# Performance work log

Measured on AMD Instinct MI355X. Metric: run time of the kernel, lower is better.

Reference implementation:

```python
import jax, jax.numpy as jnp
import numpy as np

_LN2 = 0.6931471805599453
B, N, C, R, K = 256, 4096, 256, 32, 128
MAX_SPAN = 20.0
W_WEIGHT, W_COACT, W_SPAN = 1.0, 1.0, 0.3


def setup_inputs() -> dict:
    key = jax.random.key(0)
    k1, k2, k3, k4, k5 = jax.random.split(key, 5)
    A = jax.random.normal(k1, (B, N), dtype=jnp.float32)            # accumulated atom activations
    span_t = jax.random.uniform(k2, (B,), dtype=jnp.float32) * MAX_SPAN
    proto_weights = jax.random.normal(k3, (C, N), dtype=jnp.float32) * 0.5
    proto_coact_U = jax.random.normal(k4, (C, N, R), dtype=jnp.float32) * 0.1
    proto_span = jax.random.normal(k5, (C,), dtype=jnp.float32) + 5.0
    return {"A": A, "span_t": span_t, "proto_weights": proto_weights,
            "proto_coact_U": proto_coact_U, "proto_span": proto_span}


def reference(A, span_t, proto_weights, proto_coact_U, proto_span):
    # CoActivationComputer._compute: top-K atoms per trajectory
    topk_vals, topk_idx = jax.lax.top_k(A, K)                       # [B,K], [B,K]

    # --- match_score ---
    proto_w = jax.nn.softplus(proto_weights) - _LN2                 # [C,N]
    score_w = A @ proto_w.T                                          # [B,C]
    score_w = score_w - jnp.mean(score_w, axis=1, keepdims=True)

    # CoActState.frob_inner_lowrank: gather U rows at top-k indices
    U_t = jnp.transpose(proto_coact_U, (1, 2, 0))                    # [N,R,C]
    U_topk = U_t[topk_idx]                                           # [B,K,R,C] (irregular gather)
    Au = jnp.einsum('bk,bkrc->brc', topk_vals, U_topk)               # [B,R,C]
    score_coact = jnp.sum(Au ** 2, axis=1) / (K * R + 1e-9)          # [B,C]

    span_norm = jnp.clip(span_t / MAX_SPAN, 0.0, 1.0)                # [B]
    proto_span_norm = jax.nn.sigmoid(proto_span)                     # [C]
    score_span = -jnp.abs(span_norm[:, None] - proto_span_norm[None, :])

    match_scores = W_WEIGHT * score_w + W_COACT * score_coact + W_SPAN * score_span  # [B,C]

    # --- compute_residual_score ---
    beta = jax.nn.softmax(match_scores, axis=-1)                     # [B,C]
    U_recon = jnp.einsum('bc,cnr->bnr', beta, proto_coact_U)         # [B,N,R]
    norm_Mhat = jnp.sum(topk_vals ** 2, axis=1)                      # [B]
    U_recon_topk = jnp.take_along_axis(U_recon, topk_idx[:, :, None], axis=1)  # [B,K,R]
    Au2 = jnp.einsum('bk,bkr->br', topk_vals, U_recon_topk)          # [B,R]
    cross = jnp.sum(Au2 ** 2, axis=1) / (K * R + 1e-9)
    norm_Mrecon = jnp.sum(U_recon ** 2, axis=(1, 2)) / (K * R + 1e-9)
    norm_Mhat_n = norm_Mhat / (K + 1e-9)
    residual = jnp.clip(norm_Mhat_n - 2.0 * cross + norm_Mrecon, 0.0, 10000.0)  # [B]
    return residual
```

## Files before the change

kernel.cpp:

```cpp
#include <hip/hip_runtime.h>
#include <math.h>

#define Bb 256
#define Nn 4096
#define Cc 256
#define Rr 32
#define Kk 128
#define Lflat (Nn * Rr)
#define LN2f 0.6931471805599453f
#define SKW 16

typedef unsigned short u16;
typedef __attribute__((ext_vector_type(8))) short short8b;
typedef __attribute__((ext_vector_type(4))) float f32x4;

typedef __attribute__((address_space(1))) const void* gas_t;
typedef __attribute__((address_space(3))) void* las_t;
__device__ __forceinline__ void gll16(const void* g, void* l) {
  __builtin_amdgcn_global_load_lds((gas_t)g, (las_t)l, 16, 0, 0);
}

__device__ inline u16 f2bf(float x) {
  unsigned u = __float_as_uint(x);
  unsigned r = (u + 0x7fffu + ((u >> 16) & 1u)) >> 16;
  return (u16)r;
}

__device__ inline unsigned f2u(float f) {
  unsigned b = __float_as_uint(f);
  return (b & 0x80000000u) ? ~b : (b | 0x80000000u);
}
__device__ inline float u2f(unsigned u) {
  unsigned b = (u & 0x80000000u) ? (u ^ 0x80000000u) : ~u;
  return __uint_as_float(b);
}

__global__ __launch_bounds__(256) void topk_kernel(const float* __restrict__ A,
                                                   u16* __restrict__ S,
                                                   float* __restrict__ mhat) {
  int b = blockIdx.x, t = threadIdx.x;
  int lane = t & 63, wave = t >> 6;
  const float* row = A + (size_t)b * Nn;
  u16* Srow = S + (size_t)b * Nn;
  short8b z = {0, 0, 0, 0, 0, 0, 0, 0};
  *(short8b*)(Srow + t * 16) = z;
  *(short8b*)(Srow + t * 16 + 8) = z;

  float f[16]; unsigned u[16];
#pragma unroll
  for (int j = 0; j < 4; ++j) {
    float4 v = ((const float4*)row)[j * 256 + t];
    f[j * 4 + 0] = v.x; f[j * 4 + 1] = v.y; f[j * 4 + 2] = v.z; f[j * 4 + 3] = v.w;
  }
#pragma unroll
  for (int j = 0; j < 16; ++j) u[j] = f2u(f[j]);

  __shared__ int hist[4][256];
  __shared__ int sufs[257];
  __shared__ int wtot[4];
  __shared__ int s_d, s_cg;
  __shared__ int s_eqidx[256];
  __shared__ int s_eqcnt;
  __shared__ float redQ[4];
  if (t == 0) s_eqcnt = 0;

  unsigned T = 0u;
  int cntG = 0;
#pragma unroll
  for (int p = 3; p >= 0; --p) {
    hist[0][t] = 0; hist[1][t] = 0; hist[2][t] = 0; hist[3][t] = 0;
    __syncthreads();
    unsigned mh = (p == 3) ? 0u : (0xFFFFFFFFu << (8 * (p + 1)));
    int* hw = hist[wave];
#pragma unroll
    for (int j = 0; j < 16; ++j)
      if (((u[j] ^ T) & mh) == 0) atomicAdd(&hw[(u[j] >> (8 * p)) & 255], 1);
    __syncthreads();
    int v = hist[0][t] + hist[1][t] + hist[2][t] + hist[3][t];
#pragma unroll
    for (int off = 1; off < 64; off <<= 1) {
      int tmp = __shfl_down(v, off, 64);
      if (lane + off < 64) v += tmp;
    }
    if (lane == 0) wtot[wave] = v;
    __syncthreads();
    for (int w2 = wave + 1; w2 < 4; ++w2) v += wtot[w2];
    sufs[t] = v;
    if (t == 0) sufs[256] = 0;
    __syncthreads();
    int nxt = sufs[t + 1];
    if ((cntG + v >= Kk) && (cntG + nxt < Kk)) { s_d = t; s_cg = cntG + nxt; }
    __syncthreads();
    T |= (unsigned)s_d << (8 * p);
    cntG = s_cg;
    __syncthreads();
  }
  float sq = 0.f;
#pragma unroll
  for (int j = 0; j < 16; ++j) {
    int idx = (j >> 2) * 1024 + t * 4 + (j & 3);
    if (u[j] > T) {
      Srow[idx] = f2bf(f[j]);
      sq += f[j] * f[j];
    } else if (u[j] == T) {
      int q2 = atomicAdd(&s_eqcnt, 1);
      if (q2 < 256) s_eqidx[q2] = idx;
    }
  }
#pragma unroll
  for (int off = 32; off; off >>= 1) sq += __shfl_xor(sq, off, 64);
  if (lane == 0) redQ[wave] = sq;
  __syncthreads();
  if (t == 0) {
    float tv = u2f(T);
    u16 tb = f2bf(tv);
    int need = Kk - cntG;
    int eq = min(s_eqcnt, 256);
    for (int s2 = 0; s2 < need; ++s2) {
      int best = 0x7fffffff, bi = 0;
      for (int jj = 0; jj < eq; ++jj)
        if (s_eqidx[jj] < best) { best = s_eqidx[jj]; bi = jj; }
      Srow[best] = tb;
      s_eqidx[bi] = 0x7fffffff;
    }
    mhat[b] = redQ[0] + redQ[1] + redQ[2] + redQ[3] + (float)need * tv * tv;
  }
}

__global__ __launch_bounds__(256) void u2t_kernel(const float* __restrict__ U,
                                                  u16* __restrict__ UT) {
  int c = blockIdx.x, nb = blockIdx.y, t = threadIdx.x;
  int r = t & 31, nblk = t >> 5;
  const float* Uc = U + (size_t)c * Lflat;
  u16* UTc = UT + (size_t)c * Lflat;
  for (int it = 0; it < 8; ++it) {
    int n0 = nb * 512 + it * 64 + nblk * 8;
    union { short8b v; u16 s[8]; } pk;
#pragma unroll
    for (int i = 0; i < 8; ++i)
      pk.s[i] = f2bf(Uc[(size_t)(n0 + i) * Rr + r]);
    *(short8b*)(UTc + (size_t)r * Nn + n0) = pk.v;
  }
}

__global__ __launch_bounds__(256) void scorew_mfma_kernel(const float* __restrict__ Ag,
                                                          const float* __restrict__ W,
                                                          float* __restrict__ SWp) {
  int ct = blockIdx.x, mt = blockIdx.y, ks = blockIdx.z;
  int t = threadIdx.x;
  int lane = t & 63, wave = t >> 6;
  int lo = lane & 15, hi = lane >> 4;
  int wr = wave >> 1, wc = wave & 1;
  __shared__ __align__(16) u16 As[64 * 64];
  __shared__ __align__(16) u16 Ws[64 * 64];
  f32x4 acc[2][2];
#pragma unroll
  for (int m = 0; m < 2; ++m)
#pragma unroll
    for (int n = 0; n < 2; ++n) acc[m][n] = (f32x4){0.f, 0.f, 0.f, 0.f};
  int kbase = ks * (Nn / SKW);
  for (int k0 = 0; k0 < Nn / SKW; k0 += 64) {
    for (int s = t; s < 1024; s += 256) {
      int panel = s >> 9;
      int sl = s & 511;
      int row = sl >> 3, q = sl & 7;
      union { short8b v; u16 u[8]; } pk;
      if (panel == 0) {
        const float* src = Ag + (size_t)(mt * 64 + row) * Nn + kbase + k0 + q * 8;
        float4 f0 = *(const float4*)src, f1 = *(const float4*)(src + 4);
        pk.u[0] = f2bf(f0.x); pk.u[1] = f2bf(f0.y); pk.u[2] = f2bf(f0.z); pk.u[3] = f2bf(f0.w);
        pk.u[4] = f2bf(f1.x); pk.u[5] = f2bf(f1.y); pk.u[6] = f2bf(f1.z); pk.u[7] = f2bf(f1.w);
        *(short8b*)(&As[row * 64 + ((q ^ (row & 7)) << 3)]) = pk.v;
      } else {
        const float* src = W + (size_t)(ct * 64 + row) * Nn + kbase + k0 + q * 8;
        float4 f0 = *(const float4*)src, f1 = *(const float4*)(src + 4);
        float w[8] = {f0.x, f0.y, f0.z, f0.w, f1.x, f1.y, f1.z, f1.w};
#pragma unroll
        for (int j = 0; j < 8; ++j)
          pk.u[j] = f2bf(fmaxf(w[j], 0.f) + log1pf(expf(-fabsf(w[j]))) - LN2f);
        *(short8b*)(&Ws[row * 64 + ((q ^ (row & 7)) << 3)]) = pk.v;
      }
    }
    __syncthreads();
#pragma unroll
    for (int kf = 0; kf < 2; ++kf) {
      int q = kf * 4 + hi;
      short8b af[2], bf[2];
#pragma unroll
      for (int m = 0; m < 2; ++m) {
        int row = wr * 32 + m * 16 + lo;
        af[m] = *(const short8b*)(&As[row * 64 + ((q ^ (row & 7)) << 3)]);
      }
#pragma unroll
      for (int n = 0; n < 2; ++n) {
        int row = wc * 32 + n * 16 + lo;
        bf[n] = *(const short8b*)(&Ws[row * 64 + ((q ^ (row & 7)) << 3)]);
      }
#pragma unroll
      for (int m = 0; m < 2; ++m)
#pragma unroll
        for (int n = 0; n < 2; ++n)
          acc[m][n] = __builtin_amdgcn_mfma_f32_16x16x32_bf16(af[m], bf[n], acc[m][n], 0, 0, 0);
    }
    __syncthreads();
  }
  float* o = SWp + (size_t)ks * (Bb * Cc);
#pragma unroll
  for (int m = 0; m < 2; ++m)
#pragma unroll
    for (int n = 0; n < 2; ++n)
#pragma unroll
      for (int r = 0; r < 4; ++r) {
        int b = mt * 64 + wr * 32 + m * 16 + hi * 4 + r;
        int c = ct * 64 + wc * 32 + n * 16 + lo;
        o[(size_t)b * Cc + c] = acc[m][n][r];
      }
}

__global__ __launch_bounds__(256) void gram_bf16_kernel(const u16* __restrict__ UT,
                                                        float* __restrict__ Gpart,
                                                        int kch) {
  int bx = blockIdx.x;
  int tile = bx % 3, chunk = bx / 3;
  int ti = (tile == 2) ? 1 : 0;
  int tj = (tile == 0) ? 0 : 1;
  bool diag = (tile != 1);
  int t = threadIdx.x, lane = t & 63, wave = t >> 6;
  int lo = lane & 15, hi = lane >> 4;
  int wr = wave >> 1, wc = wave & 1;
  __shared__ __align__(16) u16 lp[2][128 * 64];
  f32x4 acc[4][4];
#pragma unroll
  for (int m = 0; m < 4; ++m)
#pragma unroll
    for (int n = 0; n < 4; ++n) acc[m][n] = (f32x4){0.f, 0.f, 0.f, 0.f};
  int lrow = lane >> 3;
  int lchunk8 = ((lane & 7) ^ lrow) * 8;
  size_t kbase = (size_t)chunk * kch;
  for (int k0 = 0; k0 < kch; k0 += 64) {
    size_t kg = kbase + k0;
#pragma unroll
    for (int q = 0; q < 4; ++q) {
      int row = wave * 32 + q * 8;
      gll16(UT + (size_t)(ti * 128 + row + lrow) * Lflat + kg + lchunk8, &lp[0][row * 64]);
    }
    if (!diag) {
#pragma unroll
      for (int q = 0; q < 4; ++q) {
        int row = wave * 32 + q * 8;
        gll16(UT + (size_t)(tj * 128 + row + lrow) * Lflat + kg + lchunk8, &lp[1][row * 64]);
      }
    }
    __syncthreads();
#pragma unroll
    for (int ks = 0; ks < 2; ++ks) {
      short8b af[4], bfv[4];
#pragma unroll
      for (int m = 0; m < 4; ++m) {
        int row = wr * 64 + m * 16 + lo;
        af[m] = *(const short8b*)(&lp[0][row * 64 + (((ks * 4 + hi) ^ (row & 7)) << 3)]);
      }
      const u16* pb = diag ? lp[0] : lp[1];
#pragma unroll
      for (int n = 0; n < 4; ++n) {
        int row = wc * 64 + n * 16 + lo;
        bfv[n] = *(const short8b*)(&pb[row * 64 + (((ks * 4 + hi) ^ (row & 7)) << 3)]);
      }
#pragma unroll
      for (int m = 0; m < 4; ++m)
#pragma unroll
        for (int n = 0; n < 4; ++n)
          acc[m][n] = __builtin_amdgcn_mfma_f32_16x16x32_bf16(af[m], bfv[n], acc[m][n], 0, 0, 0);
    }
    __syncthreads();
  }
  float* gp = Gpart + (size_t)bx * 16384;
#pragma unroll
  for (int m = 0; m < 4; ++m)
#pragma unroll
    for (int n = 0; n < 4; ++n)
#pragma unroll
      for (int r = 0; r < 4; ++r) {
        int row = wr * 64 + m * 16 + hi * 4 + r;
        int col = wc * 64 + n * 16 + lo;
        gp[row * 128 + col] = acc[m][n][r];
      }
}

__global__ __launch_bounds__(256) void gram_mfma_kernel(const float* __restrict__ U,
                                                        float* __restrict__ Gpart,
                                                        int kch) {
  int bx = blockIdx.x;
  int tile = bx % 3;
  int chunk = bx / 3;
  int ti = (tile == 2) ? 1 : 0;
  int tj = (tile == 0) ? 0 : 1;
  bool diag = (tile != 1);
  int t = threadIdx.x;
  int lane = t & 63, wave = t >> 6;
  int lo = lane & 15, hi = lane >> 4;
  int wr = wave >> 1, wc = wave & 1;
  __shared__ __align__(16) u16 lp[2][128 * 64];
  size_t kbase = (size_t)chunk * kch;
  f32x4 acc[4][4];
#pragma unroll
  for (int m = 0; m < 4; ++m)
#pragma unroll
    for (int n = 0; n < 4; ++n) acc[m][n] = (f32x4){0.f, 0.f, 0.f, 0.f};
  int nslots = diag ? 1024 : 2048;
  for (int k0 = 0; k0 < kch; k0 += 64) {
    for (int s = t; s < nslots; s += 256) {
      int panel = s >> 10;
      int sl = s & 1023;
      int row = sl >> 3, q = sl & 7;
      int grow = (panel ? tj : ti) * 128 + row;
      const float* src = U + (size_t)grow * Lflat + kbase + k0 + q * 8;
      float4 f0 = *(const float4*)src;
      float4 f1 = *(const float4*)(src + 4);
      union { short8b v; u16 u[8]; } pk;
      pk.u[0] = f2bf(f0.x); pk.u[1] = f2bf(f0.y); pk.u[2] = f2bf(f0.z); pk.u[3] = f2bf(f0.w);
      pk.u[4] = f2bf(f1.x); pk.u[5] = f2bf(f1.y); pk.u[6] = f2bf(f1.z); pk.u[7] = f2bf(f1.w);
      *(short8b*)(&lp[panel][row * 64 + ((q ^ (row & 7)) << 3)]) = pk.v;
    }
    __syncthreads();
#pragma unroll
    for (int ks = 0; ks < 2; ++ks) {
      short8b af[4], bfv[4];
#pragma unroll
      for (int m = 0; m < 4; ++m) {
        int row = wr * 64 + m * 16 + lo;
        af[m] = *(const short8b*)(&lp[0][row * 64 + (((ks * 4 + hi) ^ (row & 7)) << 3)]);
      }
      const u16* pb = diag ? lp[0] : lp[1];
#pragma unroll
      for (int n = 0; n < 4; ++n) {
        int row = wc * 64 + n * 16 + lo;
        bfv[n] = *(const short8b*)(&pb[row * 64 + (((ks * 4 + hi) ^ (row & 7)) << 3)]);
      }
#pragma unroll
      for (int m = 0; m < 4; ++m)
#pragma unroll
        for (int n = 0; n < 4; ++n)
          acc[m][n] = __builtin_amdgcn_mfma_f32_16x16x32_bf16(af[m], bfv[n], acc[m][n], 0, 0, 0);
    }
    __syncthreads();
  }
  float* gp = Gpart + (size_t)bx * 16384;
#pragma unroll
  for (int m = 0; m < 4; ++m)
#pragma unroll
    for (int n = 0; n < 4; ++n)
#pragma unroll
      for (int r = 0; r < 4; ++r) {
        int row = wr * 64 + m * 16 + hi * 4 + r;
        int col = wc * 64 + n * 16 + lo;
        gp[row * 128 + col] = acc[m][n][r];
      }
}

__global__ __launch_bounds__(256) void gram_reduce_kernel(const float* __restrict__ Gpart,
                                                          float* __restrict__ G,
                                                          int nchunks) {
  int tile = blockIdx.x % 3, seg = blockIdx.x / 3;
  int ti = (tile == 2) ? 1 : 0;
  int tj = (tile == 0) ? 0 : 1;
  int e = seg * 1024 + threadIdx.x * 4;
  float4 s = {0.f, 0.f, 0.f, 0.f};
  for (int ch = 0; ch < nchunks; ++ch) {
    float4 v = *(const float4*)(Gpart + ((size_t)(ch * 3 + tile)) * 16384 + e);
    s.x += v.x; s.y += v.y; s.z += v.z; s.w += v.w;
  }
  int row = e >> 7, col = e & 127;
  int gi = ti * 128 + row, gj = tj * 128 + col;
  G[gi * Cc + gj + 0] = s.x;
  G[gi * Cc + gj + 1] = s.y;
  G[gi * Cc + gj + 2] = s.z;
  G[gi * Cc + gj + 3] = s.w;
  if (tile == 1) {
    G[(gj + 0) * Cc + gi] = s.x;
    G[(gj + 1) * Cc + gi] = s.y;
    G[(gj + 2) * Cc + gi] = s.z;
    G[(gj + 3) * Cc + gi] = s.w;
  }
}

__global__ __launch_bounds__(256) void au_gemm_kernel(const u16* __restrict__ S,
                                                      const u16* __restrict__ UT,
                                                      float* __restrict__ Au,
                                                      float* __restrict__ SC) {
  int jt = blockIdx.x, bt = blockIdx.y;
  int t = threadIdx.x, lane = t & 63, wave = t >> 6;
  int lo = lane & 15, hi = lane >> 4;
  int wr = wave >> 1, wc = wave & 1;
  __shared__ __align__(16) u16 Sa[128 * 64];
  __shared__ __align__(16) u16 Ub[64 * 64];
  f32x4 acc[4][2];
#pragma unroll
  for (int m = 0; m < 4; ++m)
#pragma unroll
    for (int n = 0; n < 2; ++n) acc[m][n] = (f32x4){0.f, 0.f, 0.f, 0.f};
  int lrow = lane >> 3;
  int lchunk8 = ((lane & 7) ^ lrow) * 8;
  for (int k0 = 0; k0 < Nn; k0 += 64) {
#pragma unroll
    for (int q = 0; q < 4; ++q) {
      int row = wave * 32 + q * 8;
      gll16(S + (size_t)(bt * 128 + row + lrow) * Nn + k0 + lchunk8, &Sa[row * 64]);
    }
#pragma unroll
    for (int q = 0; q < 2; ++q) {
      int row = wave * 16 + q * 8;
      gll16(UT + (size_t)(jt * 64 + row + lrow) * Nn + k0 + lchunk8, &Ub[row * 64]);
    }
    __syncthreads();
#pragma unroll
    for (int ks = 0; ks < 2; ++ks) {
      int q = ks * 4 + hi;
      short8b af[4], bfv[2];
#pragma unroll
      for (int m = 0; m < 4; ++m) {
        int r = wr * 64 + m * 16 + lo;
        af[m] = *(const short8b*)(&Sa[r * 64 + ((q ^ (r & 7)) << 3)]);
      }
#pragma unroll
      for (int n = 0; n < 2; ++n) {
        int r = wc * 32 + n * 16 + lo;
        bfv[n] = *(const short8b*)(&Ub[r * 64 + ((q ^ (r & 7)) << 3)]);
      }
#pragma unroll
      for (int m = 0; m < 4; ++m)
#pragma unroll
        for (int n = 0; n < 2; ++n)
          acc[m][n] = __builtin_amdgcn_mfma_f32_16x16x32_bf16(af[m], bfv[n], acc[m][n], 0, 0, 0);
    }
    __syncthreads();
  }
  int c = jt * 2 + wc;
#pragma unroll
  for (int m = 0; m < 4; ++m)
#pragma unroll
    for (int rr = 0; rr < 4; ++rr) {
      int b = bt * 128 + wr * 64 + m * 16 + hi * 4 + rr;
      float a0 = acc[m][0][rr], a1 = acc[m][1][rr];
      Au[((size_t)b * Cc + c) * Rr + lo]      = a0;
      Au[((size_t)b * Cc + c) * Rr + 16 + lo] = a1;
      float sq = a0 * a0 + a1 * a1;
      sq += __shfl_xor(sq, 1, 64);
      sq += __shfl_xor(sq, 2, 64);
      sq += __shfl_xor(sq, 4, 64);
      sq += __shfl_xor(sq, 8, 64);
      if (lo == 0) SC[(size_t)b * Cc + c] = sq * (1.f / (Kk * Rr));
    }
}

__global__ __launch_bounds__(256) void au_mfma_kernel(const float* __restrict__ U,
                                                      const u16* __restrict__ S,
                                                      float* __restrict__ Au,
                                                      float* __restrict__ SC) {
  int c = blockIdx.x, mb = blockIdx.y;
  int t = threadIdx.x;
  int lane = t & 63, wave = t >> 6;
  int lo = lane & 15, hi = lane >> 4;
  __shared__ __align__(16) u16 Ss[128 * 64];
  __shared__ __align__(16) u16 Us[32 * 64];
  f32x4 acc[2][2];
#pragma unroll
  for (int m = 0; m < 2; ++m)
#pragma unroll
    for (int n = 0; n < 2; ++n) acc[m][n] = (f32x4){0.f, 0.f, 0.f, 0.f};
  const float* Uc = U + (size_t)c * Lflat;
  for (int k0 = 0; k0 < Nn; k0 += 64) {
    for (int s = t; s < 1024; s += 256) {
      int row = s >> 3, q = s & 7;
      short8b v = *(const short8b*)(S + (size_t)(mb * 128 + row) * Nn + k0 + q * 8);
      *(short8b*)(&Ss[row * 64 + ((q ^ (row & 7)) << 3)]) = v;
    }
    for (int s = t; s < 512; s += 256) {
      int kk = s >> 3, rq = s & 7;
      float4 f = *(const float4*)(Uc + (size_t)(k0 + kk) * Rr + rq * 4);
      float fv[4] = {f.x, f.y, f.z, f.w};
#pragma unroll
      for (int j = 0; j < 4; ++j) {
        int r = rq * 4 + j;
        Us[r * 64 + (((kk >> 3) ^ (r & 7)) << 3) + (kk & 7)] = f2bf(fv[j]);
      }
    }
    __syncthreads();
#pragma unroll
    for (int kf = 0; kf < 2; ++kf) {
      int q = kf * 4 + hi;
      short8b af[2], bf[2];
#pragma unroll
      for (int m = 0; m < 2; ++m) {
        int row = wave * 32 + m * 16 + lo;
        af[m] = *(const short8b*)(&Ss[row * 64 + ((q ^ (row & 7)) << 3)]);
      }
#pragma unroll
      for (int n = 0; n < 2; ++n) {
        int row = n * 16 + lo;
        bf[n] = *(const short8b*)(&Us[row * 64 + ((q ^ (row & 7)) << 3)]);
      }
#pragma unroll
      for (int m = 0; m < 2; ++m)
#pragma unroll
        for (int n = 0; n < 2; ++n)
          acc[m][n] = __builtin_amdgcn_mfma_f32_16x16x32_bf16(af[m], bf[n], acc[m][n], 0, 0, 0);
    }
    __syncthreads();
  }
#pragma unroll
  for (int m = 0; m < 2; ++m) {
#pragma unroll
    for (int r = 0; r < 4; ++r) {
      int b = mb * 128 + wave * 32 + m * 16 + hi * 4 + r;
#pragma unroll
      for (int n = 0; n < 2; ++n) {
        int rr = n * 16 + lo;
        Au[((size_t)b * Cc + c) * Rr + rr] = acc[m][n][r];
      }
      float sq = acc[m][0][r] * acc[m][0][r] + acc[m][1][r] * acc[m][1][r];
      sq += __shfl_xor(sq, 1, 64);
      sq += __shfl_xor(sq, 2, 64);
      sq += __shfl_xor(sq, 4, 64);
      sq += __shfl_xor(sq, 8, 64);
      if (lo == 0) SC[(size_t)b * Cc + c] = sq * (1.f / (Kk * Rr));
    }
  }
}

__global__ __launch_bounds__(256) void softfin_kernel(const float* __restrict__ SWp,
                                                      const float* __restrict__ SC,
                                                      const float* __restrict__ span_t,
                                                      const float* __restrict__ PS,
                                                      const float* __restrict__ G,
                                                      const float* __restrict__ Au,
                                                      const float* __restrict__ mhat,
                                                      float* __restrict__ out) {
  int b = blockIdx.x, t = threadIdx.x;
  int lane = t & 63, wave = t >> 6;
  __shared__ float redM[4], redS[4], redA[4];
  __shared__ float sb[Cc];
  __shared__ float au2[8][32];
  float span_norm = fminf(fmaxf(span_t[b] * (1.f / 20.f), 0.f), 1.f);
  float psn = 1.f / (1.f + expf(-PS[t]));
  float m = 0.f;
#pragma unroll
  for (int kc = 0; kc < SKW; ++kc) m += SWp[(size_t)kc * (Bb * Cc) + b * Cc + t];
  m += SC[b * Cc + t] - 0.3f * fabsf(span_norm - psn);
  float mx = m;
#pragma unroll
  for (int off = 32; off; off >>= 1) mx = fmaxf(mx, __shfl_xor(mx, off, 64));
  if (lane == 0) redM[wave] = mx;
  __syncthreads();
  mx = fmaxf(fmaxf(redM[0], redM[1]), fmaxf(redM[2], redM[3]));
  float e = expf(m - mx);
  float s = e;
#pragma unroll
  for (int off = 32; off; off >>= 1) s += __shfl_xor(s, off, 64);
  if (lane == 0) redS[wave] = s;
  __syncthreads();
  s = redS[0] + redS[1] + redS[2] + redS[3];
  float beta_t = e / s;
  sb[t] = beta_t;
  __syncthreads();
  float w = 0.f;
#pragma unroll 8
  for (int c = 0; c < Cc; ++c) w = fmaf(sb[c], G[c * Cc + t], w);
  float pr = beta_t * w;
  int r = t & 31, g = t >> 5;
  float pp = 0.f;
#pragma unroll 8
  for (int cc = 0; cc < 32; ++cc) {
    int c = cc * 8 + g;
    pp = fmaf(sb[c], Au[((size_t)b * Cc + c) * Rr + r], pp);
  }
  au2[g][r] = pp;
  float x = pr;
#pragma unroll
  for (int off = 32; off; off >>= 1) x += __shfl_xor(x, off, 64);
  if (lane == 0) redA[wave] = x;
  __syncthreads();
  float recon = (redA[0] + redA[1] + redA[2] + redA[3]) * (1.f / 4096.f);
  float cr = 0.f;
  if (t < 32) {
    float a2 = au2[0][t] + au2[1][t] + au2[2][t] + au2[3][t]
             + au2[4][t] + au2[5][t] + au2[6][t] + au2[7][t];
    cr = a2 * a2;
  }
#pragma unroll
  for (int off = 16; off; off >>= 1) cr += __shfl_xor(cr, off, 64);
  if (t == 0) {
    cr *= (1.f / 4096.f);
    float res = mhat[b] * (1.f / 128.f) - 2.f * cr + recon;
    out[b] = fminf(fmaxf(res, 0.f), 10000.f);
  }
}

extern "C" void kernel_launch(void* const* d_in, const int* in_sizes, int n_in,
                              void* d_out, int out_size, void* d_ws, size_t ws_size,
                              hipStream_t stream) {
  const float* A      = (const float*)d_in[0];
  const float* span_t = (const float*)d_in[1];
  const float* W      = (const float*)d_in[2];
  const float* U      = (const float*)d_in[3];
  const float* PS     = (const float*)d_in[4];
  float* out = (float*)d_out;

  char* p = (char*)d_ws;
  float* mhat = (float*)p; p += (size_t)Bb * 4;
  float* SWp  = (float*)p; p += (size_t)SKW * Bb * Cc * 4;
  float* SC   = (float*)p; p += (size_t)Bb * Cc * 4;
  float* G    = (float*)p; p += (size_t)Cc * Cc * 4;
  u16*   S    = (u16*)p;   p += (size_t)Bb * Nn * 2;
  float* Au   = (float*)p; p += (size_t)Bb * Cc * Rr * 4;
  size_t fixed = (size_t)(p - (char*)d_ws);
  size_t UTsz = (size_t)Cc * Lflat * 2;
  bool planA = ws_size >= fixed + UTsz + (size_t)3 * 8 * 16384 * 4;

  topk_kernel<<<dim3(Bb), dim3(256), 0, stream>>>(A, S, mhat);
  scorew_mfma_kernel<<<dim3(4, 4, SKW), dim3(256), 0, stream>>>(A, W, SWp);

  if (planA) {
    u16* UT = (u16*)p; p += UTsz;
    size_t used = fixed + UTsz;
    int nchunks = 64;
    while (nchunks > 8 && used + (size_t)(3 * nchunks) * 16384 * 4 > ws_size) nchunks >>= 1;
    float* Gpart = (float*)p;
    u2t_kernel<<<dim3(Cc, 8), dim3(256), 0, stream>>>(U, UT);
    gram_bf16_kernel<<<dim3(3 * nchunks), dim3(256), 0, stream>>>(UT, Gpart, Lflat / nchunks);
    gram_reduce_kernel<<<dim3(48), dim3(256), 0, stream>>>(Gpart, G, nchunks);
    au_gemm_kernel<<<dim3(128, 2), dim3(256), 0, stream>>>(S, UT, Au, SC);
  } else {
    int nchunks = 64;
    while (nchunks > 8 && fixed + (size_t)(3 * nchunks) * 16384 * 4 > ws_size) nchunks >>= 1;
    float* Gpart = (float*)p;
    gram_mfma_kernel<<<dim3(3 * nchunks), dim3(256), 0, stream>>>(U, Gpart, Lflat / nchunks);
    gram_reduce_kernel<<<dim3(48), dim3(256), 0, stream>>>(Gpart, G, nchunks);
    au_mfma_kernel<<<dim3(Cc, 2), dim3(256), 0, stream>>>(U, S, Au, SC);
  }

  softfin_kernel<<<dim3(Bb), dim3(256), 0, stream>>>(SWp, SC, span_t, PS, G, Au, mhat, out);
}
```

Before: 193.3 us.

## Merge independent kernels into two block-dispatched megakernels and retile Au GEMM

Folds the U transpose/bf16 conversion, top-k selection and score_w GEMM into one launch whose blocks dispatch by block index. The Au GEMM and the Gram partial GEMM are likewise merged into a second launch. The Au GEMM tile is widened to 128x128 with half as many blocks, and the Gram split count goes from 64 to 128 chunks. This cuts launch count and the idle tail between small kernels so independent work can run concurrently. The cost is heterogeneous blocks sharing one register and LDS budget, and more Gram partials for the reduce step to sum.

New measurement: 194.3 us. Within noise of the previous version (+0.5%).

```diff
diff --git a/kernel.cpp b/kernel.cpp
--- a/kernel.cpp
+++ b/kernel.cpp
@@ -35,256 +35,346 @@
   return __uint_as_float(b);
 }
 
-__global__ __launch_bounds__(256) void topk_kernel(const float* __restrict__ A,
-                                                   u16* __restrict__ S,
-                                                   float* __restrict__ mhat) {
-  int b = blockIdx.x, t = threadIdx.x;
-  int lane = t & 63, wave = t >> 6;
-  const float* row = A + (size_t)b * Nn;
-  u16* Srow = S + (size_t)b * Nn;
-  short8b z = {0, 0, 0, 0, 0, 0, 0, 0};
-  *(short8b*)(Srow + t * 16) = z;
-  *(short8b*)(Srow + t * 16 + 8) = z;
-
-  float f[16]; unsigned u[16];
-#pragma unroll
-  for (int j = 0; j < 4; ++j) {
-    float4 v = ((const float4*)row)[j * 256 + t];
-    f[j * 4 + 0] = v.x; f[j * 4 + 1] = v.y; f[j * 4 + 2] = v.z; f[j * 4 + 3] = v.w;
-  }
-#pragma unroll
-  for (int j = 0; j < 16; ++j) u[j] = f2u(f[j]);
-
-  __shared__ int hist[4][256];
-  __shared__ int sufs[257];
-  __shared__ int wtot[4];
-  __shared__ int s_d, s_cg;
-  __shared__ int s_eqidx[256];
-  __shared__ int s_eqcnt;
-  __shared__ float redQ[4];
-  if (t == 0) s_eqcnt = 0;
-
-  unsigned T = 0u;
-  int cntG = 0;
-#pragma unroll
-  for (int p = 3; p >= 0; --p) {
-    hist[0][t] = 0; hist[1][t] = 0; hist[2][t] = 0; hist[3][t] = 0;
+struct TopkSh {
+  int hist[4][256];
+  int sufs[257];
+  int wtot[4];
+  int s_d, s_cg;
+  int eqidx[256];
+  int eqcnt;
+  float redQ[4];
+};
+
+__global__ __launch_bounds__(256) void mega1_kernel(const float* __restrict__ A,
+                                                    const float* __restrict__ W,
+                                                    const float* __restrict__ U,
+                                                    u16* __restrict__ S,
+                                                    float* __restrict__ mhat,
+                                                    u16* __restrict__ UT,
+                                                    float* __restrict__ SWp,
+                                                    int ofs) {
+  extern __shared__ __align__(16) char smem[];
+  int bid = blockIdx.x + ofs;
+  int t = threadIdx.x;
+
+  if (bid < 2048) {
+    int c = bid >> 3, nb = bid & 7;
+    int r = t & 31, nblk = t >> 5;
+    const float* Uc = U + (size_t)c * Lflat;
+    u16* UTc = UT + (size_t)c * Lflat;
+    for (int it = 0; it < 8; ++it) {
+      int n0 = nb * 512 + it * 64 + nblk * 8;
+      union { short8b v; u16 s[8]; } pk;
+#pragma unroll
+      for (int i = 0; i < 8; ++i)
+        pk.s[i] = f2bf(Uc[(size_t)(n0 + i) * Rr + r]);
+      *(short8b*)(UTc + (size_t)r * Nn + n0) = pk.v;
+    }
+    return;
+  }
+
+  if (bid < 2304) {
+    TopkSh* sh = (TopkSh*)smem;
+    int b = bid - 2048;
+    int lane = t & 63, wave = t >> 6;
+    const float* row = A + (size_t)b * Nn;
+    u16* Srow = S + (size_t)b * Nn;
+    short8b z = {0, 0, 0, 0, 0, 0, 0, 0};
+    *(short8b*)(Srow + t * 16) = z;
+    *(short8b*)(Srow + t * 16 + 8) = z;
+
+    float f[16]; unsigned u[16];
+#pragma unroll
+    for (int j = 0; j < 4; ++j) {
+      float4 v = ((const float4*)row)[j * 256 + t];
+      f[j * 4 + 0] = v.x; f[j * 4 + 1] = v.y; f[j * 4 + 2] = v.z; f[j * 4 + 3] = v.w;
+    }
+#pragma unroll
+    for (int j = 0; j < 16; ++j) u[j] = f2u(f[j]);
+
+    if (t == 0) sh->eqcnt = 0;
+    unsigned T = 0u;
+    int cntG = 0;
+#pragma unroll
+    for (int p = 3; p >= 0; --p) {
+      sh->hist[0][t] = 0; sh->hist[1][t] = 0; sh->hist[2][t] = 0; sh->hist[3][t] = 0;
+      __syncthreads();
+      unsigned mh = (p == 3) ? 0u : (0xFFFFFFFFu << (8 * (p + 1)));
+      int* hw = sh->hist[wave];
+#pragma unroll
+      for (int j = 0; j < 16; ++j)
+        if (((u[j] ^ T) & mh) == 0) atomicAdd(&hw[(u[j] >> (8 * p)) & 255], 1);
+      __syncthreads();
+      int v = sh->hist[0][t] + sh->hist[1][t] + sh->hist[2][t] + sh->hist[3][t];
+#pragma unroll
+      for (int off = 1; off < 64; off <<= 1) {
+        int tmp = __shfl_down(v, off, 64);
+        if (lane + off < 64) v += tmp;
+      }
+      if (lane == 0) sh->wtot[wave] = v;
+      __syncthreads();
+      for (int w2 = wave + 1; w2 < 4; ++w2) v += sh->wtot[w2];
+      sh->sufs[t] = v;
+      if (t == 0) sh->sufs[256] = 0;
+      __syncthreads();
+      int nxt = sh->sufs[t + 1];
+      if ((cntG + v >= Kk) && (cntG + nxt < Kk)) { sh->s_d = t; sh->s_cg = cntG + nxt; }
+      __syncthreads();
+      T |= (unsigned)sh->s_d << (8 * p);
+      cntG = sh->s_cg;
+      __syncthreads();
+    }
+    float sq = 0.f;
+#pragma unroll
+    for (int j = 0; j < 16; ++j) {
+      int idx = (j >> 2) * 1024 + t * 4 + (j & 3);
+      if (u[j] > T) {
+        Srow[idx] = f2bf(f[j]);
+        sq += f[j] * f[j];
+      } else if (u[j] == T) {
+        int q2 = atomicAdd(&sh->eqcnt, 1);
+        if (q2 < 256) sh->eqidx[q2] = idx;
+      }
+    }
+#pragma unroll
+    for (int off = 32; off; off >>= 1) sq += __shfl_xor(sq, off, 64);
+    if (lane == 0) sh->redQ[wave] = sq;
     __syncthreads();
-    unsigned mh = (p == 3) ? 0u : (0xFFFFFFFFu << (8 * (p + 1)));
-    int* hw = hist[wave];
-#pragma unroll
-    for (int j = 0; j < 16; ++j)
-      if (((u[j] ^ T) & mh) == 0) atomicAdd(&hw[(u[j] >> (8 * p)) & 255], 1);
-    __syncthreads();
-    int v = hist[0][t] + hist[1][t] + hist[2][t] + hist[3][t];
-#pragma unroll
-    for (int off = 1; off < 64; off <<= 1) {
-      int tmp = __shfl_down(v, off, 64);
-      if (lane + off < 64) v += tmp;
-    }
-    if (lane == 0) wtot[wave] = v;
-    __syncthreads();
-    for (int w2 = wave + 1; w2 < 4; ++w2) v += wtot[w2];
-    sufs[t] = v;
-    if (t == 0) sufs[256] = 0;
-    __syncthreads();
-    int nxt = sufs[t + 1];
-    if ((cntG + v >= Kk) && (cntG + nxt < Kk)) { s_d = t; s_cg = cntG + nxt; }
-    __syncthreads();
-    T |= (unsigned)s_d << (8 * p);
-    cntG = s_cg;
-    __syncthreads();
-  }
-  float sq = 0.f;
-#pragma unroll
-  for (int j = 0; j < 16; ++j) {
-    int idx = (j >> 2) * 1024 + t * 4 + (j & 3);
-    if (u[j] > T) {
-      Srow[idx] = f2bf(f[j]);
-      sq += f[j] * f[j];
-    } else if (u[j] == T) {
-      int q2 = atomicAdd(&s_eqcnt, 1);
-      if (q2 < 256) s_eqidx[q2] = idx;
-    }
-  }
-#pragma unroll
-  for (int off = 32; off; off >>= 1) sq += __shfl_xor(sq, off, 64);
-  if (lane == 0) redQ[wave] = sq;
-  __syncthreads();
-  if (t == 0) {
-    float tv = u2f(T);
-    u16 tb = f2bf(tv);
-    int need = Kk - cntG;
-    int eq = min(s_eqcnt, 256);
-    for (int s2 = 0; s2 < need; ++s2) {
-      int best = 0x7fffffff, bi = 0;
-      for (int jj = 0; jj < eq; ++jj)
-        if (s_eqidx[jj] < best) { best = s_eqidx[jj]; bi = jj; }
-      Srow[best] = tb;
-      s_eqidx[bi] = 0x7fffffff;
-    }
-    mhat[b] = redQ[0] + redQ[1] + redQ[2] + redQ[3] + (float)need * tv * tv;
-  }
-}
-
-__global__ __launch_bounds__(256) void u2t_kernel(const float* __restrict__ U,
-                                                  u16* __restrict__ UT) {
-  int c = blockIdx.x, nb = blockIdx.y, t = threadIdx.x;
-  int r = t & 31, nblk = t >> 5;
-  const float* Uc = U + (size_t)c * Lflat;
-  u16* UTc = UT + (size_t)c * Lflat;
-  for (int it = 0; it < 8; ++it) {
-    int n0 = nb * 512 + it * 64 + nblk * 8;
-    union { short8b v; u16 s[8]; } pk;
-#pragma unroll
-    for (int i = 0; i < 8; ++i)
-      pk.s[i] = f2bf(Uc[(size_t)(n0 + i) * Rr + r]);
-    *(short8b*)(UTc + (size_t)r * Nn + n0) = pk.v;
-  }
-}
-
-__global__ __launch_bounds__(256) void scorew_mfma_kernel(const float* __restrict__ Ag,
-                                                          const float* __restrict__ W,
-                                                          float* __restrict__ SWp) {
-  int ct = blockIdx.x, mt = blockIdx.y, ks = blockIdx.z;
-  int t = threadIdx.x;
-  int lane = t & 63, wave = t >> 6;
-  int lo = lane & 15, hi = lane >> 4;
-  int wr = wave >> 1, wc = wave & 1;
-  __shared__ __align__(16) u16 As[64 * 64];
-  __shared__ __align__(16) u16 Ws[64 * 64];
-  f32x4 acc[2][2];
-#pragma unroll
-  for (int m = 0; m < 2; ++m)
-#pragma unroll
-    for (int n = 0; n < 2; ++n) acc[m][n] = (f32x4){0.f, 0.f, 0.f, 0.f};
-  int kbase = ks * (Nn / SKW);
-  for (int k0 = 0; k0 < Nn / SKW; k0 += 64) {
-    for (int s = t; s < 1024; s += 256) {
-      int panel = s >> 9;
-      int sl = s & 511;
-      int row = sl >> 3, q = sl & 7;
-      union { short8b v; u16 u[8]; } pk;
-      if (panel == 0) {
-        const float* src = Ag + (size_t)(mt * 64 + row) * Nn + kbase + k0 + q * 8;
-        float4 f0 = *(const float4*)src, f1 = *(const float4*)(src + 4);
-        pk.u[0] = f2bf(f0.x); pk.u[1] = f2bf(f0.y); pk.u[2] = f2bf(f0.z); pk.u[3] = f2bf(f0.w);
-        pk.u[4] = f2bf(f1.x); pk.u[5] = f2bf(f1.y); pk.u[6] = f2bf(f1.z); pk.u[7] = f2bf(f1.w);
-        *(short8b*)(&As[row * 64 + ((q ^ (row & 7)) << 3)]) = pk.v;
-      } else {
-        const float* src = W + (size_t)(ct * 64 + row) * Nn + kbase + k0 + q * 8;
-        float4 f0 = *(const float4*)src, f1 = *(const float4*)(src + 4);
-        float w[8] = {f0.x, f0.y, f0.z, f0.w, f1.x, f1.y, f1.z, f1.w};
-#pragma unroll
-        for (int j = 0; j < 8; ++j)
-          pk.u[j] = f2bf(fmaxf(w[j], 0.f) + log1pf(expf(-fabsf(w[j]))) - LN2f);
-        *(short8b*)(&Ws[row * 64 + ((q ^ (row & 7)) << 3)]) = pk.v;
-      }
-    }
-    __syncthreads();
-#pragma unroll
-    for (int kf = 0; kf < 2; ++kf) {
-      int q = kf * 4 + hi;
-      short8b af[2], bf[2];
-#pragma unroll
-      for (int m = 0; m < 2; ++m) {
-        int row = wr * 32 + m * 16 + lo;
-        af[m] = *(const short8b*)(&As[row * 64 + ((q ^ (row & 7)) << 3)]);
-      }
-#pragma unroll
-      for (int n = 0; n < 2; ++n) {
-        int row = wc * 32 + n * 16 + lo;
-        bf[n] = *(const short8b*)(&Ws[row * 64 + ((q ^ (row & 7)) << 3)]);
-      }
-#pragma unroll
-      for (int m = 0; m < 2; ++m)
-#pragma unroll
-        for (int n = 0; n < 2; ++n)
-          acc[m][n] = __builtin_amdgcn_mfma_f32_16x16x32_bf16(af[m], bf[n], acc[m][n], 0, 0, 0);
-    }
-    __syncthreads();
-  }
-  float* o = SWp + (size_t)ks * (Bb * Cc);
-#pragma unroll
-  for (int m = 0; m < 2; ++m)
-#pragma unroll
-    for (int n = 0; n < 2; ++n)
-#pragma unroll
-      for (int r = 0; r < 4; ++r) {
-        int b = mt * 64 + wr * 32 + m * 16 + hi * 4 + r;
-        int c = ct * 64 + wc * 32 + n * 16 + lo;
-        o[(size_t)b * Cc + c] = acc[m][n][r];
-      }
-}
-
-__global__ __launch_bounds__(256) void gram_bf16_kernel(const u16* __restrict__ UT,
-                                                        float* __restrict__ Gpart,
-                                                        int kch) {
-  int bx = blockIdx.x;
-  int tile = bx % 3, chunk = bx / 3;
-  int ti = (tile == 2) ? 1 : 0;
-  int tj = (tile == 0) ? 0 : 1;
-  bool diag = (tile != 1);
+    if (t == 0) {
+      float tv = u2f(T);
+      u16 tb = f2bf(tv);
+      int need = Kk - cntG;
+      int eq = min(sh->eqcnt, 256);
+      for (int s2 = 0; s2 < need; ++s2) {
+        int best = 0x7fffffff, bi = 0;
+        for (int jj = 0; jj < eq; ++jj)
+          if (sh->eqidx[jj] < best) { best = sh->eqidx[jj]; bi = jj; }
+        Srow[best] = tb;
+        sh->eqidx[bi] = 0x7fffffff;
+      }
+      mhat[b] = sh->redQ[0] + sh->redQ[1] + sh->redQ[2] + sh->redQ[3] + (float)need * tv * tv;
+    }
+    return;
+  }
+
+  {
+    u16* As = (u16*)smem;
+    u16* Ws = (u16*)(smem + 8192);
+    int idx = bid - 2304;
+    int ct = idx & 3, mt = (idx >> 2) & 3, ks = idx >> 4;
+    int lane = t & 63, wave = t >> 6;
+    int lo = lane & 15, hi = lane >> 4;
+    int wr = wave >> 1, wc = wave & 1;
+    f32x4 acc[2][2];
+#pragma unroll
+    for (int m = 0; m < 2; ++m)
+#pragma unroll
+      for (int n = 0; n < 2; ++n) acc[m][n] = (f32x4){0.f, 0.f, 0.f, 0.f};
+    int kbase = ks * (Nn / SKW);
+    for (int k0 = 0; k0 < Nn / SKW; k0 += 64) {
+      for (int s = t; s < 1024; s += 256) {
+        int panel = s >> 9;
+        int sl = s & 511;
+        int row = sl >> 3, q = sl & 7;
+        union { short8b v; u16 u[8]; } pk;
+        if (panel == 0) {
+          const float* src = A + (size_t)(mt * 64 + row) * Nn + kbase + k0 + q * 8;
+          float4 f0 = *(const float4*)src, f1 = *(const float4*)(src + 4);
+          pk.u[0] = f2bf(f0.x); pk.u[1] = f2bf(f0.y); pk.u[2] = f2bf(f0.z); pk.u[3] = f2bf(f0.w);
+          pk.u[4] = f2bf(f1.x); pk.u[5] = f2bf(f1.y); pk.u[6] = f2bf(f1.z); pk.u[7] = f2bf(f1.w);
+          *(short8b*)(&As[row * 64 + ((q ^ (row & 7)) << 3)]) = pk.v;
+        } else {
+          const float* src = W + (size_t)(ct * 64 + row) * Nn + kbase + k0 + q * 8;
+          float4 f0 = *(const float4*)src, f1 = *(const float4*)(src + 4);
+          float w[8] = {f0.x, f0.y, f0.z, f0.w, f1.x, f1.y, f1.z, f1.w};
+#pragma unroll
+          for (int j = 0; j < 8; ++j)
+            pk.u[j] = f2bf(fmaxf(w[j], 0.f) + log1pf(expf(-fabsf(w[j]))) - LN2f);
+          *(short8b*)(&Ws[row * 64 + ((q ^ (row & 7)) << 3)]) = pk.v;
+        }
+      }
+      __syncthreads();
+#pragma unroll
+      for (int kf = 0; kf < 2; ++kf) {
+        int q = kf * 4 + hi;
+        short8b af[2], bf[2];
+#pragma unroll
+        for (int m = 0; m < 2; ++m) {
+          int row = wr * 32 + m * 16 + lo;
+          af[m] = *(const short8b*)(&As[row * 64 + ((q ^ (row & 7)) << 3)]);
+        }
+#pragma unroll
+        for (int n = 0; n < 2; ++n) {
+          int row = wc * 32 + n * 16 + lo;
+          bf[n] = *(const short8b*)(&Ws[row * 64 + ((q ^ (row & 7)) << 3)]);
+        }
+#pragma unroll
+        for (int m = 0; m < 2; ++m)
+#pragma unroll
+          for (int n = 0; n < 2; ++n)
+            acc[m][n] = __builtin_amdgcn_mfma_f32_16x16x32_bf16(af[m], bf[n], acc[m][n], 0, 0, 0);
+      }
+      __syncthreads();
+    }
+    float* o = SWp + (size_t)ks * (Bb * Cc);
+#pragma unroll
+    for (int m = 0; m < 2; ++m)
+#pragma unroll
+      for (int n = 0; n < 2; ++n)
+#pragma unroll
+        for (int r = 0; r < 4; ++r) {
+          int b = mt * 64 + wr * 32 + m * 16 + hi * 4 + r;
+          int c = ct * 64 + wc * 32 + n * 16 + lo;
+          o[(size_t)b * Cc + c] = acc[m][n][r];
+        }
+  }
+}
+
+__global__ __launch_bounds__(256) void mega2_kernel(const u16* __restrict__ S,
+                                                    const u16* __restrict__ UT,
+                                                    float* __restrict__ Au,
+                                                    float* __restrict__ SC,
+                                                    float* __restrict__ Gpart,
+                                                    int kch) {
+  extern __shared__ __align__(16) char smem[];
+  int bid = blockIdx.x;
   int t = threadIdx.x, lane = t & 63, wave = t >> 6;
   int lo = lane & 15, hi = lane >> 4;
   int wr = wave >> 1, wc = wave & 1;
-  __shared__ __align__(16) u16 lp[2][128 * 64];
-  f32x4 acc[4][4];
-#pragma unroll
-  for (int m = 0; m < 4; ++m)
-#pragma unroll
-    for (int n = 0; n < 4; ++n) acc[m][n] = (f32x4){0.f, 0.f, 0.f, 0.f};
   int lrow = lane >> 3;
   int lchunk8 = ((lane & 7) ^ lrow) * 8;
-  size_t kbase = (size_t)chunk * kch;
-  for (int k0 = 0; k0 < kch; k0 += 64) {
-    size_t kg = kbase + k0;
-#pragma unroll
-    for (int q = 0; q < 4; ++q) {
-      int row = wave * 32 + q * 8;
-      gll16(UT + (size_t)(ti * 128 + row + lrow) * Lflat + kg + lchunk8, &lp[0][row * 64]);
-    }
-    if (!diag) {
+
+  if (bid < 128) {
+    int jt = bid & 63, bt = bid >> 6;
+    u16* Sa = (u16*)smem;
+    u16* Ub = (u16*)(smem + 16384);
+    f32x4 acc[4][4];
+#pragma unroll
+    for (int m = 0; m < 4; ++m)
+#pragma unroll
+      for (int n = 0; n < 4; ++n) acc[m][n] = (f32x4){0.f, 0.f, 0.f, 0.f};
+    for (int k0 = 0; k0 < Nn; k0 += 64) {
 #pragma unroll
       for (int q = 0; q < 4; ++q) {
         int row = wave * 32 + q * 8;
-        gll16(UT + (size_t)(tj * 128 + row + lrow) * Lflat + kg + lchunk8, &lp[1][row * 64]);
-      }
-    }
-    __syncthreads();
-#pragma unroll
-    for (int ks = 0; ks < 2; ++ks) {
-      short8b af[4], bfv[4];
-#pragma unroll
-      for (int m = 0; m < 4; ++m) {
-        int row = wr * 64 + m * 16 + lo;
-        af[m] = *(const short8b*)(&lp[0][row * 64 + (((ks * 4 + hi) ^ (row & 7)) << 3)]);
-      }
-      const u16* pb = diag ? lp[0] : lp[1];
-#pragma unroll
-      for (int n = 0; n < 4; ++n) {
-        int row = wc * 64 + n * 16 + lo;
-        bfv[n] = *(const short8b*)(&pb[row * 64 + (((ks * 4 + hi) ^ (row & 7)) << 3)]);
-      }
-#pragma unroll
-      for (int m = 0; m < 4; ++m)
-#pragma unroll
-        for (int n = 0; n < 4; ++n)
-          acc[m][n] = __builtin_amdgcn_mfma_f32_16x16x32_bf16(af[m], bfv[n], acc[m][n], 0, 0, 0);
-    }
-    __syncthreads();
-  }
-  float* gp = Gpart + (size_t)bx * 16384;
-#pragma unroll
-  for (int m = 0; m < 4; ++m)
-#pragma unroll
-    for (int n = 0; n < 4; ++n)
-#pragma unroll
-      for (int r = 0; r < 4; ++r) {
-        int row = wr * 64 + m * 16 + hi * 4 + r;
-        int col = wc * 64 + n * 16 + lo;
-        gp[row * 128 + col] = acc[m][n][r];
-      }
+        gll16(S + (size_t)(bt * 128 + row + lrow) * Nn + k0 + lchunk8, &Sa[row * 64]);
+        gll16(UT + (size_t)(jt * 128 + row + lrow) * Nn + k0 + lchunk8, &Ub[row * 64]);
+      }
+      __syncthreads();
+#pragma unroll
+      for (int ks = 0; ks < 2; ++ks) {
+        int q = ks * 4 + hi;
+        short8b af[4], bfv[4];
+#pragma unroll
+        for (int m = 0; m < 4; ++m) {
+          int r = wr * 64 + m * 16 + lo;
+          af[m] = *(const short8b*)(&Sa[r * 64 + ((q ^ (r & 7)) << 3)]);
+        }
+#pragma unroll
+        for (int n = 0; n < 4; ++n) {
+          int r = wc * 64 + n * 16 + lo;
+          bfv[n] = *(const short8b*)(&Ub[r * 64 + ((q ^ (r & 7)) << 3)]);
+        }
+#pragma unroll
+        for (int m = 0; m < 4; ++m)
+#pragma unroll
+          for (int n = 0; n < 4; ++n)
+            acc[m][n] = __builtin_amdgcn_mfma_f32_16x16x32_bf16(af[m], bfv[n], acc[m][n], 0, 0, 0);
+      }
+      __syncthreads();
+    }
+#pragma unroll
+    for (int m = 0; m < 4; ++m)
+#pragma unroll
+      for (int rr = 0; rr < 4; ++rr) {
+        int b = bt * 128 + wr * 64 + m * 16 + hi * 4 + rr;
+#pragma unroll
+        for (int n = 0; n < 4; ++n) {
+          int col = wc * 64 + n * 16 + lo;
+          int c = jt * 4 + (col >> 5);
+          int r = col & 31;
+          Au[((size_t)b * Cc + c) * Rr + r] = acc[m][n][rr];
+        }
+#pragma unroll
+        for (int cp = 0; cp < 2; ++cp) {
+          float a0 = acc[m][2 * cp][rr], a1 = acc[m][2 * cp + 1][rr];
+          float sq = a0 * a0 + a1 * a1;
+          sq += __shfl_xor(sq, 1, 64);
+          sq += __shfl_xor(sq, 2, 64);
+          sq += __shfl_xor(sq, 4, 64);
+          sq += __shfl_xor(sq, 8, 64);
+          if (lo == 0) {
+            int c = jt * 4 + wc * 2 + cp;
+            SC[(size_t)b * Cc + c] = sq * (1.f / (Kk * Rr));
+          }
+        }
+      }
+    return;
+  }
+
+  {
+    int idx = bid - 128;
+    int tile = idx % 3, chunk = idx / 3;
+    int ti = (tile == 2) ? 1 : 0;
+    int tj = (tile == 0) ? 0 : 1;
+    bool diag = (tile != 1);
+    u16* lp0 = (u16*)smem;
+    u16* lp1 = (u16*)(smem + 16384);
+    f32x4 acc[4][4];
+#pragma unroll
+    for (int m = 0; m < 4; ++m)
+#pragma unroll
+      for (int n = 0; n < 4; ++n) acc[m][n] = (f32x4){0.f, 0.f, 0.f, 0.f};
+    size_t kbase = (size_t)chunk * kch;
+    for (int k0 = 0; k0 < kch; k0 += 64) {
+      size_t kg = kbase + k0;
+#pragma unroll
+      for (int q = 0; q < 4; ++q) {
+        int row = wave * 32 + q * 8;
+        gll16(UT + (size_t)(ti * 128 + row + lrow) * Lflat + kg + lchunk8, &lp0[row * 64]);
+      }
+      if (!diag) {
+#pragma unroll
+        for (int q = 0; q < 4; ++q) {
+          int row = wave * 32 + q * 8;
+          gll16(UT + (size_t)(tj * 128 + row + lrow) * Lflat + kg + lchunk8, &lp1[row * 64]);
+        }
+      }
+      __syncthreads();
+#pragma unroll
+      for (int ks = 0; ks < 2; ++ks) {
+        short8b af[4], bfv[4];
+#pragma unroll
+        for (int m = 0; m < 4; ++m) {
+          int row = wr * 64 + m * 16 + lo;
+          af[m] = *(const short8b*)(&lp0[row * 64 + (((ks * 4 + hi) ^ (row & 7)) << 3)]);
+        }
+        const u16* pb = diag ? lp0 : lp1;
+#pragma unroll
+        for (int n = 0; n < 4; ++n) {
+          int row = wc * 64 + n * 16 + lo;
+          bfv[n] = *(const short8b*)(&pb[row * 64 + (((ks * 4 + hi) ^ (row & 7)) << 3)]);
+        }
+#pragma unroll
+        for (int m = 0; m < 4; ++m)
+#pragma unroll
+          for (int n = 0; n < 4; ++n)
+            acc[m][n] = __builtin_amdgcn_mfma_f32_16x16x32_bf16(af[m], bfv[n], acc[m][n], 0, 0, 0);
+      }
+      __syncthreads();
+    }
+    float* gp = Gpart + (size_t)idx * 16384;
+#pragma unroll
+    for (int m = 0; m < 4; ++m)
+#pragma unroll
+      for (int n = 0; n < 4; ++n)
+#pragma unroll
+        for (int r = 0; r < 4; ++r) {
+          int row = wr * 64 + m * 16 + hi * 4 + r;
+          int col = wc * 64 + n * 16 + lo;
+          gp[row * 128 + col] = acc[m][n][r];
+        }
+  }
 }
 
 __global__ __launch_bounds__(256) void gram_mfma_kernel(const float* __restrict__ U,
@@ -382,75 +472,6 @@
     G[(gj + 2) * Cc + gi] = s.z;
     G[(gj + 3) * Cc + gi] = s.w;
   }
-}
-
-__global__ __launch_bounds__(256) void au_gemm_kernel(const u16* __restrict__ S,
-                                                      const u16* __restrict__ UT,
-                                                      float* __restrict__ Au,
-                                                      float* __restrict__ SC) {
-  int jt = blockIdx.x, bt = blockIdx.y;
-  int t = threadIdx.x, lane = t & 63, wave = t >> 6;
-  int lo = lane & 15, hi = lane >> 4;
-  int wr = wave >> 1, wc = wave & 1;
-  __shared__ __align__(16) u16 Sa[128 * 64];
-  __shared__ __align__(16) u16 Ub[64 * 64];
-  f32x4 acc[4][2];
-#pragma unroll
-  for (int m = 0; m < 4; ++m)
-#pragma unroll
-    for (int n = 0; n < 2; ++n) acc[m][n] = (f32x4){0.f, 0.f, 0.f, 0.f};
-  int lrow = lane >> 3;
-  int lchunk8 = ((lane & 7) ^ lrow) * 8;
-  for (int k0 = 0; k0 < Nn; k0 += 64) {
-#pragma unroll
-    for (int q = 0; q < 4; ++q) {
-      int row = wave * 32 + q * 8;
-      gll16(S + (size_t)(bt * 128 + row + lrow) * Nn + k0 + lchunk8, &Sa[row * 64]);
-    }
-#pragma unroll
-    for (int q = 0; q < 2; ++q) {
-      int row = wave * 16 + q * 8;
-      gll16(UT + (size_t)(jt * 64 + row + lrow) * Nn + k0 + lchunk8, &Ub[row * 64]);
-    }
-    __syncthreads();
-#pragma unroll
-    for (int ks = 0; ks < 2; ++ks) {
-      int q = ks * 4 + hi;
-      short8b af[4], bfv[2];
-#pragma unroll
-      for (int m = 0; m < 4; ++m) {
-        int r = wr * 64 + m * 16 + lo;
-        af[m] = *(const short8b*)(&Sa[r * 64 + ((q ^ (r & 7)) << 3)]);
-      }
-#pragma unroll
-      for (int n = 0; n < 2; ++n) {
-        int r = wc * 32 + n * 16 + lo;
-        bfv[n] = *(const short8b*)(&Ub[r * 64 + ((q ^ (r & 7)) << 3)]);
-      }
-#pragma unroll
-      for (int m = 0; m < 4; ++m)
-#pragma unroll
-        for (int n = 0; n < 2; ++n)
-          acc[m][n] = __builtin_amdgcn_mfma_f32_16x16x32_bf16(af[m], bfv[n], acc[m][n], 0, 0, 0);
-    }
-    __syncthreads();
-  }
-  int c = jt * 2 + wc;
-#pragma unroll
-  for (int m = 0; m < 4; ++m)
-#pragma unroll
-    for (int rr = 0; rr < 4; ++rr) {
-      int b = bt * 128 + wr * 64 + m * 16 + hi * 4 + rr;
-      float a0 = acc[m][0][rr], a1 = acc[m][1][rr];
-      Au[((size_t)b * Cc + c) * Rr + lo]      = a0;
-      Au[((size_t)b * Cc + c) * Rr + 16 + lo] = a1;
-      float sq = a0 * a0 + a1 * a1;
-      sq += __shfl_xor(sq, 1, 64);
-      sq += __shfl_xor(sq, 2, 64);
-      sq += __shfl_xor(sq, 4, 64);
-      sq += __shfl_xor(sq, 8, 64);
-      if (lo == 0) SC[(size_t)b * Cc + c] = sq * (1.f / (Kk * Rr));
-    }
 }
 
 __global__ __launch_bounds__(256) void au_mfma_kernel(const float* __restrict__ U,
@@ -617,23 +638,21 @@
   size_t UTsz = (size_t)Cc * Lflat * 2;
   bool planA = ws_size >= fixed + UTsz + (size_t)3 * 8 * 16384 * 4;
 
-  topk_kernel<<<dim3(Bb), dim3(256), 0, stream>>>(A, S, mhat);
-  scorew_mfma_kernel<<<dim3(4, 4, SKW), dim3(256), 0, stream>>>(A, W, SWp);
-
   if (planA) {
     u16* UT = (u16*)p; p += UTsz;
     size_t used = fixed + UTsz;
-    int nchunks = 64;
+    int nchunks = 128;
     while (nchunks > 8 && used + (size_t)(3 * nchunks) * 16384 * 4 > ws_size) nchunks >>= 1;
     float* Gpart = (float*)p;
-    u2t_kernel<<<dim3(Cc, 8), dim3(256), 0, stream>>>(U, UT);
-    gram_bf16_kernel<<<dim3(3 * nchunks), dim3(256), 0, stream>>>(UT, Gpart, Lflat / nchunks);
+    mega1_kernel<<<dim3(2560), dim3(256), 16384, stream>>>(A, W, U, S, mhat, UT, SWp, 0);
+    mega2_kernel<<<dim3(128 + 3 * nchunks), dim3(256), 32768, stream>>>(S, UT, Au, SC, Gpart,
+                                                                        Lflat / nchunks);
     gram_reduce_kernel<<<dim3(48), dim3(256), 0, stream>>>(Gpart, G, nchunks);
-    au_gemm_kernel<<<dim3(128, 2), dim3(256), 0, stream>>>(S, UT, Au, SC);
   } else {
     int nchunks = 64;
     while (nchunks > 8 && fixed + (size_t)(3 * nchunks) * 16384 * 4 > ws_size) nchunks >>= 1;
     float* Gpart = (float*)p;
+    mega1_kernel<<<dim3(512), dim3(256), 16384, stream>>>(A, W, U, S, mhat, nullptr, SWp, 2048);
     gram_mfma_kernel<<<dim3(3 * nchunks), dim3(256), 0, stream>>>(U, Gpart, Lflat / nchunks);
     gram_reduce_kernel<<<dim3(48), dim3(256), 0, stream>>>(Gpart, G, nchunks);
     au_mfma_kernel<<<dim3(Cc, 2), dim3(256), 0, stream>>>(U, S, Au, SC);
```
